# Kernel optimization log

Hardware: AMD Instinct MI355X
Metric: run time of the kernel (lower is better)

Reference implementation:

```python
import jax, jax.numpy as jnp
import numpy as np
from jax.scipy.special import logsumexp

T, B, H, K = 256, 256, 512, 64


def setup_inputs() -> dict:
    key = jax.random.key(0)
    k1, k2, k3, k4, k5, k6, k7, k8 = jax.random.split(key, 8)
    hiddens = jax.random.normal(k1, (T, B, H), dtype=jnp.float32)
    lens = jax.random.randint(k2, (B,), 1, T + 1)              # sentence lengths in [1, T]
    tags = jax.random.randint(k3, (T, B), 0, K)                # gold tags
    W = jax.random.normal(k4, (K, H), dtype=jnp.float32) * (1.0 / np.sqrt(H))
    b = jax.random.normal(k5, (K,), dtype=jnp.float32) * 0.01
    begin_transition = jax.random.normal(k6, (K,), dtype=jnp.float32)
    transition = jax.random.normal(k7, (K, K), dtype=jnp.float32)
    end_transition = jax.random.normal(k8, (K,), dtype=jnp.float32)
    return {"hiddens": hiddens, "lens": lens, "tags": tags, "W": W, "b": b,
            "begin_transition": begin_transition, "transition": transition,
            "end_transition": end_transition}


def reference(hiddens, lens, tags, W, b, begin_transition, transition, end_transition):
    # emissions: [T, B, K] = hidden2emission(hiddens)
    em = jnp.einsum('tbh,kh->tbk', hiddens, W) + b
    t_len, batch, k = em.shape

    # ---- forward (partition) score: log-semiring DP over time ----
    alpha0 = em[0] + begin_transition                       # [B, K]

    def step(alpha, e_t):
        # alpha_t[b, j] = logsumexp_i(alpha[b, i] + transition[j, i]) + e_t[b, j]
        a = logsumexp(alpha[:, None, :] + transition[None, :, :], axis=-1) + e_t
        return a, a

    _, alphas = jax.lax.scan(step, alpha0, em[1:])          # [T-1, B, K]
    alphas = jnp.concatenate([alpha0[None], alphas], axis=0)  # [T, B, K]

    bidx = jnp.arange(batch)
    last_alpha = alphas[lens - 1, bidx]                     # [B, K] at each sentence end
    forward_score = logsumexp(last_alpha + end_transition, axis=-1)  # [B]

    # ---- gold path score ----
    em_g = jnp.take_along_axis(em, tags[:, :, None], axis=-1)[..., 0]   # [T, B]
    inc = transition[tags[1:], tags[:-1]] + em_g[1:]                     # [T-1, B]
    first = (begin_transition[tags[0]] + em_g[0])[None]                  # [1, B]
    scores = jnp.cumsum(jnp.concatenate([first, inc], axis=0), axis=0)   # [T, B]
    last_scores = scores[lens - 1, bidx]                                 # [B]
    last_tags = tags[lens - 1, bidx]
    gold_score = last_scores + end_transition[last_tags]                 # [B]

    return jnp.sum(forward_score - gold_score)
```

## Files before the change

kernel.cpp:

```cpp
#include <hip/hip_runtime.h>
#include <hip/hip_bf16.h>
#include <math.h>

#define T_DIM 256
#define B_DIM 256
#define H_DIM 512
#define K_DIM 64
#define LN2F 0.69314718055994531f

typedef __attribute__((ext_vector_type(8))) short bfrag_t;
typedef __attribute__((ext_vector_type(4))) float f4_t;

__device__ inline bfrag_t pack8(float4 a, float4 b) {
  union { bfrag_t v; __hip_bfloat162 h[4]; } u;
  u.h[0] = __float22bfloat162_rn(float2{a.x, a.y});
  u.h[1] = __float22bfloat162_rn(float2{a.z, a.w});
  u.h[2] = __float22bfloat162_rn(float2{b.x, b.y});
  u.h[3] = __float22bfloat162_rn(float2{b.z, b.w});
  return u.v;
}

__global__ __launch_bounds__(256) void wconv(const float* __restrict__ W,
                                             short* __restrict__ Wb,
                                             float* __restrict__ out) {
  if (blockIdx.x == 0 && threadIdx.x == 0) *out = 0.f;
  const int i = (blockIdx.x * 256 + threadIdx.x) * 8;
  const float4 a = *(const float4*)(W + i);
  const float4 b = *(const float4*)(W + i + 4);
  *(bfrag_t*)(Wb + i) = pack8(a, b);
}

__global__ __launch_bounds__(256, 4) void emis_gemm10(
    const float* __restrict__ hid,
    const short* __restrict__ Wb,
    const float* __restrict__ bias,
    const int*   __restrict__ tags,
    short* __restrict__ emPb,
    float* __restrict__ goldRaw)
{
  __shared__ __hip_bfloat16 AsH[2][64 * 72];
  float* Cs = (float*)&AsH[0][0];

  const int tid  = threadIdx.x;
  const int wv   = tid >> 6;
  const int lane = tid & 63;
  const int l16  = lane & 15;
  const int quad = lane >> 4;
  const int m0   = blockIdx.x * 64;

  const short* wb = Wb + ((wv * 16 + l16) * H_DIM + quad * 8);

  const int sr = tid >> 2;
  const int sc = (tid & 3) << 4;
  const float* hrow = hid + (size_t)(m0 + sr) * H_DIM + sc;

  f4_t acc[4];
#pragma unroll
  for (int mt = 0; mt < 4; ++mt) acc[mt] = (f4_t){0.f, 0.f, 0.f, 0.f};

  float4 p0 = *(const float4*)(hrow + 0);
  float4 p1 = *(const float4*)(hrow + 4);
  float4 p2 = *(const float4*)(hrow + 8);
  float4 p3 = *(const float4*)(hrow + 12);
  bfrag_t bc0 = *(const bfrag_t*)(wb + 0);
  bfrag_t bc1 = *(const bfrag_t*)(wb + 32);
  *(bfrag_t*)(&AsH[0][sr * 72 + sc + 0]) = pack8(p0, p1);
  *(bfrag_t*)(&AsH[0][sr * 72 + sc + 8]) = pack8(p2, p3);
  __syncthreads();

#pragma unroll
  for (int it = 0; it < 8; ++it) {
    bfrag_t bn0, bn1;
    if (it < 7) {
      p0 = *(const float4*)(hrow + (it + 1) * 64 + 0);
      p1 = *(const float4*)(hrow + (it + 1) * 64 + 4);
      p2 = *(const float4*)(hrow + (it + 1) * 64 + 8);
      p3 = *(const float4*)(hrow + (it + 1) * 64 + 12);
      bn0 = *(const bfrag_t*)(wb + (it + 1) * 64);
      bn1 = *(const bfrag_t*)(wb + (it + 1) * 64 + 32);
    }
#pragma unroll
    for (int kc2 = 0; kc2 < 2; ++kc2) {
      const bfrag_t bf = kc2 ? bc1 : bc0;
#pragma unroll
      for (int mt = 0; mt < 4; ++mt) {
        const bfrag_t af =
            *(const bfrag_t*)(&AsH[it & 1][(mt * 16 + l16) * 72 + kc2 * 32 + quad * 8]);
        acc[mt] = __builtin_amdgcn_mfma_f32_16x16x32_bf16(af, bf, acc[mt], 0, 0, 0);
      }
    }
    if (it < 7) {
      *(bfrag_t*)(&AsH[(it + 1) & 1][sr * 72 + sc + 0]) = pack8(p0, p1);
      *(bfrag_t*)(&AsH[(it + 1) & 1][sr * 72 + sc + 8]) = pack8(p2, p3);
      bc0 = bn0; bc1 = bn1;
    }
    __syncthreads();
  }

  const float bn = bias[wv * 16 + l16];
#pragma unroll
  for (int mt = 0; mt < 4; ++mt)
#pragma unroll
    for (int r = 0; r < 4; ++r)
      Cs[(mt * 16 + quad * 4 + r) * 68 + wv * 16 + l16] = acc[mt][r] + bn;
  __syncthreads();

  const int t  = m0 >> 8;
  const int b0 = m0 & 255;
  if (tid < 64) {
    const int tg = tags[t * B_DIM + b0 + tid];
    goldRaw[t * B_DIM + b0 + tid] = Cs[tid * 68 + tg];
  }

  const int g0 = b0 >> 4;
  const int bl = tid & 15;
  const int qq = (tid >> 4) & 3;
  const int gl = tid >> 6;
#pragma unroll
  for (int i2 = 0; i2 < 2; ++i2) {
    float4 v0 = *(const float4*)(&Cs[(gl * 16 + bl) * 68 + (i2 * 2 + 0) * 16 + qq * 4]);
    float4 v1 = *(const float4*)(&Cs[(gl * 16 + bl) * 68 + (i2 * 2 + 1) * 16 + qq * 4]);
    v0.x = __expf(v0.x); v0.y = __expf(v0.y); v0.z = __expf(v0.z); v0.w = __expf(v0.w);
    v1.x = __expf(v1.x); v1.y = __expf(v1.y); v1.z = __expf(v1.z); v1.w = __expf(v1.w);
    const size_t off = ((((size_t)(g0 + gl) * 256 + t) * 64 + qq * 16 + bl) << 4) + i2 * 8;
    *(bfrag_t*)(emPb + off) = pack8(v0, v1);
  }
}

__global__ __launch_bounds__(128, 1) void crf_dp10(
    const short* __restrict__ emPb,
    const float* __restrict__ goldRaw,
    const int* __restrict__ lens,
    const int* __restrict__ tags,
    const float* __restrict__ trans,
    const float* __restrict__ beginT,
    const float* __restrict__ endT,
    float* __restrict__ out)
{
  const int g    = blockIdx.x;
  const int tid  = threadIdx.x;
  const int wv   = tid >> 6;
  const int lane = tid & 63;
  const int n    = lane & 15;
  const int q    = lane >> 4;
  const int b    = g * 16 + n;

  __shared__ float xs[64 * 16];
  __shared__ int   Lxs[64];
  __shared__ float s0d[16];
  __shared__ int   Ls0[16];
  __shared__ float gpart;

  const int len = lens[b];
  const int cap = len - 1;
  const short* base = emPb + (((size_t)g * 256) * 64 + lane) * 16;

  float eend[16];
#pragma unroll
  for (int k = 0; k < 16; ++k)
    eend[k] = __expf(endT[(k >> 2) * 16 + q * 4 + (k & 3)]);

  float y[16];
  int Lint = 0;
  bfrag_t bf0, bf1;
  bfrag_t wA0, wA1, wB0, wB1, wC0, wC1, wD0, wD1;
  bfrag_t wE0, wE1, wF0, wF1, wG0, wG1, wH0, wH1;
  float g0 = 0.f;

#define LOADW(D0, D1, t) { \
    D0 = *(const bfrag_t*)(base + (size_t)(t) * 1024 + 0); \
    D1 = *(const bfrag_t*)(base + (size_t)(t) * 1024 + 8); }

#define CVT16(DST, S0, S1) { \
    union { bfrag_t v; __hip_bfloat162 h[4]; } _c0, _c1; \
    _c0.v = (S0); _c1.v = (S1); \
    float2 _f; \
    _f = __bfloat1622float2(_c0.h[0]); DST[0] = _f.x; DST[1] = _f.y; \
    _f = __bfloat1622float2(_c0.h[1]); DST[2] = _f.x; DST[3] = _f.y; \
    _f = __bfloat1622float2(_c0.h[2]); DST[4] = _f.x; DST[5] = _f.y; \
    _f = __bfloat1622float2(_c0.h[3]); DST[6] = _f.x; DST[7] = _f.y; \
    _f = __bfloat1622float2(_c1.h[0]); DST[8] = _f.x; DST[9] = _f.y; \
    _f = __bfloat1622float2(_c1.h[1]); DST[10] = _f.x; DST[11] = _f.y; \
    _f = __bfloat1622float2(_c1.h[2]); DST[12] = _f.x; DST[13] = _f.y; \
    _f = __bfloat1622float2(_c1.h[3]); DST[14] = _f.x; DST[15] = _f.y; }

#define RESCALE() { \
    float _m0 = fmaxf(fmaxf(y[0], y[1]), fmaxf(y[2], y[3])); \
    float _m1 = fmaxf(fmaxf(y[4], y[5]), fmaxf(y[6], y[7])); \
    float _m2 = fmaxf(fmaxf(y[8], y[9]), fmaxf(y[10], y[11])); \
    float _m3 = fmaxf(fmaxf(y[12], y[13]), fmaxf(y[14], y[15])); \
    float _mx = fmaxf(fmaxf(_m0, _m1), fmaxf(_m2, _m3)); \
    _mx = fmaxf(_mx, __shfl_xor(_mx, 16)); \
    _mx = fmaxf(_mx, __shfl_xor(_mx, 32)); \
    int _e; (void)frexpf(_mx, &_e); \
    Lint += _e; \
    _Pragma("unroll") for (int k = 0; k < 16; ++k) y[k] = ldexpf(y[k], -_e); }

#define BUILDBV(S) { \
    union { bfrag_t v; __hip_bfloat162 h[4]; } _u0, _u1; \
    _u0.h[0] = __float22bfloat162_rn(float2{S[0], S[1]}); \
    _u0.h[1] = __float22bfloat162_rn(float2{S[2], S[3]}); \
    _u0.h[2] = __float22bfloat162_rn(float2{S[4], S[5]}); \
    _u0.h[3] = __float22bfloat162_rn(float2{S[6], S[7]}); \
    _u1.h[0] = __float22bfloat162_rn(float2{S[8], S[9]}); \
    _u1.h[1] = __float22bfloat162_rn(float2{S[10], S[11]}); \
    _u1.h[2] = __float22bfloat162_rn(float2{S[12], S[13]}); \
    _u1.h[3] = __float22bfloat162_rn(float2{S[14], S[15]}); \
    bf0 = _u0.v; bf1 = _u1.v; }

  const f4_t zro = (f4_t){0.f, 0.f, 0.f, 0.f};

  if (wv == 0) {
    bfrag_t aE[8];
#pragma unroll
    for (int jt = 0; jt < 4; ++jt)
#pragma unroll
      for (int kt = 0; kt < 2; ++kt) {
        union { bfrag_t v; __hip_bfloat16 h[8]; } u;
#pragma unroll
        for (int r = 0; r < 8; ++r) {
          const int i = (2 * kt + (r >> 2)) * 16 + q * 4 + (r & 3);
          u.h[r] = __float2bfloat16(__expf(trans[(jt * 16 + n) * K_DIM + i]));
        }
        aE[jt * 2 + kt] = u.v;
      }

    float snap[16];
    int Lsnap = 0;
    LOADW(wA0, wA1, 0);
    {
      float w0[16];
      CVT16(w0, wA0, wA1);
#pragma unroll
      for (int k = 0; k < 16; ++k) {
        const int j = (k >> 2) * 16 + q * 4 + (k & 3);
        y[k] = w0[k] * __expf(beginT[j]);
        snap[k] = (cap == 0) ? y[k] : 0.0f;
      }
    }
    RESCALE(); BUILDBV(y);
    LOADW(wA0, wA1, 1); LOADW(wB0, wB1, 2); LOADW(wC0, wC1, 3); LOADW(wD0, wD1, 4);
    LOADW(wE0, wE1, 5); LOADW(wF0, wF1, 6); LOADW(wG0, wG1, 7); LOADW(wH0, wH1, 8);

#define STEPF(T, W0, W1, RSC) { \
    float _w[16]; \
    CVT16(_w, W0, W1); \
    f4_t _a0 = __builtin_amdgcn_mfma_f32_16x16x32_bf16(aE[0], bf0, zro, 0, 0, 0); \
    f4_t _a1 = __builtin_amdgcn_mfma_f32_16x16x32_bf16(aE[2], bf0, zro, 0, 0, 0); \
    f4_t _a2 = __builtin_amdgcn_mfma_f32_16x16x32_bf16(aE[4], bf0, zro, 0, 0, 0); \
    f4_t _a3 = __builtin_amdgcn_mfma_f32_16x16x32_bf16(aE[6], bf0, zro, 0, 0, 0); \
    _a0 = __builtin_amdgcn_mfma_f32_16x16x32_bf16(aE[1], bf1, _a0, 0, 0, 0); \
    _a1 = __builtin_amdgcn_mfma_f32_16x16x32_bf16(aE[3], bf1, _a1, 0, 0, 0); \
    _a2 = __builtin_amdgcn_mfma_f32_16x16x32_bf16(aE[5], bf1, _a2, 0, 0, 0); \
    _a3 = __builtin_amdgcn_mfma_f32_16x16x32_bf16(aE[7], bf1, _a3, 0, 0, 0); \
    _Pragma("unroll") for (int r = 0; r < 4; ++r) { \
      y[r]      = _a0[r] * _w[r]; \
      y[4 + r]  = _a1[r] * _w[4 + r]; \
      y[8 + r]  = _a2[r] * _w[8 + r]; \
      y[12 + r] = _a3[r] * _w[12 + r]; } \
    const bool _hit = ((T) == cap); \
    _Pragma("unroll") for (int k = 0; k < 16; ++k) snap[k] = _hit ? y[k] : snap[k]; \
    Lsnap = _hit ? Lint : Lsnap; \
    if (RSC) { RESCALE(); } \
    BUILDBV(y); }

    int t = 1;
    for (int it = 0; it < 15; ++it, t += 8) {
      STEPF(t + 0, wA0, wA1, 0); LOADW(wA0, wA1, t + 8);
      STEPF(t + 1, wB0, wB1, 0); LOADW(wB0, wB1, t + 9);
      STEPF(t + 2, wC0, wC1, 1); LOADW(wC0, wC1, t + 10);
      STEPF(t + 3, wD0, wD1, 0); LOADW(wD0, wD1, t + 11);
      STEPF(t + 4, wE0, wE1, 0); LOADW(wE0, wE1, t + 12);
      STEPF(t + 5, wF0, wF1, 0); LOADW(wF0, wF1, t + 13);
      STEPF(t + 6, wG0, wG1, 1); LOADW(wG0, wG1, t + 14);
      STEPF(t + 7, wH0, wH1, 0); LOADW(wH0, wH1, t + 15);
    }
    STEPF(121, wA0, wA1, 0); STEPF(122, wB0, wB1, 0); STEPF(123, wC0, wC1, 1);
    STEPF(124, wD0, wD1, 0); STEPF(125, wE0, wE1, 0); STEPF(126, wF0, wF1, 0);
    STEPF(127, wG0, wG1, 0);

#pragma unroll
    for (int k = 0; k < 16; ++k) xs[lane * 16 + k] = y[k];
    Lxs[lane] = Lint;
    float sd = 0.f;
#pragma unroll
    for (int k = 0; k < 16; ++k) sd += snap[k] * eend[k];
    sd += __shfl_xor(sd, 16);
    sd += __shfl_xor(sd, 32);
    if (lane < 16) { s0d[lane] = sd; Ls0[lane] = Lsnap; }

    for (int c = 0; c < 32; ++c) {
      const int tt = q + 4 * c;
      if (tt < len) {
        const int tg = tags[(size_t)tt * B_DIM + b];
        float v = goldRaw[(size_t)tt * B_DIM + b];
        v += (tt == 0) ? beginT[tg]
                       : trans[(size_t)tg * K_DIM + tags[(size_t)(tt - 1) * B_DIM + b]];
        if (tt == cap) v += endT[tg];
        g0 += v;
      }
    }
    float gr = g0;
#pragma unroll
    for (int o = 1; o < 64; o <<= 1) gr += __shfl_xor(gr, o);
    if (lane == 0) gpart = gr;
  } else {
    bfrag_t aET[8];
#pragma unroll
    for (int jt = 0; jt < 4; ++jt)
#pragma unroll
      for (int kt = 0; kt < 2; ++kt) {
        union { bfrag_t v; __hip_bfloat16 h[8]; } u;
#pragma unroll
        for (int r = 0; r < 8; ++r) {
          const int i = (2 * kt + (r >> 2)) * 16 + q * 4 + (r & 3);
          u.h[r] = __float2bfloat16(__expf(trans[(size_t)i * K_DIM + (jt * 16 + n)]));
        }
        aET[jt * 2 + kt] = u.v;
      }

#pragma unroll
    for (int k = 0; k < 16; ++k) y[k] = 0.f;
    LOADW(wA0, wA1, 255); LOADW(wB0, wB1, 254); LOADW(wC0, wC1, 253); LOADW(wD0, wD1, 252);
    LOADW(wE0, wE1, 251); LOADW(wF0, wF1, 250); LOADW(wG0, wG1, 249); LOADW(wH0, wH1, 248);

#define STEPB(T, W0, W1, RSC) { \
    float _w[16]; \
    CVT16(_w, W0, W1); \
    const bool _hit = ((T) == cap); \
    float _d[16]; \
    _Pragma("unroll") for (int k = 0; k < 16; ++k) \
      _d[k] = (_hit ? eend[k] : y[k]) * _w[k]; \
    BUILDBV(_d); \
    f4_t _a0 = __builtin_amdgcn_mfma_f32_16x16x32_bf16(aET[0], bf0, zro, 0, 0, 0); \
    f4_t _a1 = __builtin_amdgcn_mfma_f32_16x16x32_bf16(aET[2], bf0, zro, 0, 0, 0); \
    f4_t _a2 = __builtin_amdgcn_mfma_f32_16x16x32_bf16(aET[4], bf0, zro, 0, 0, 0); \
    f4_t _a3 = __builtin_amdgcn_mfma_f32_16x16x32_bf16(aET[6], bf0, zro, 0, 0, 0); \
    _a0 = __builtin_amdgcn_mfma_f32_16x16x32_bf16(aET[1], bf1, _a0, 0, 0, 0); \
    _a1 = __builtin_amdgcn_mfma_f32_16x16x32_bf16(aET[3], bf1, _a1, 0, 0, 0); \
    _a2 = __builtin_amdgcn_mfma_f32_16x16x32_bf16(aET[5], bf1, _a2, 0, 0, 0); \
    _a3 = __builtin_amdgcn_mfma_f32_16x16x32_bf16(aET[7], bf1, _a3, 0, 0, 0); \
    _Pragma("unroll") for (int r = 0; r < 4; ++r) { \
      y[r]      = _a0[r]; \
      y[4 + r]  = _a1[r]; \
      y[8 + r]  = _a2[r]; \
      y[12 + r] = _a3[r]; } \
    if (RSC) { RESCALE(); } }

    int t = 255;
    for (int it = 0; it < 16; ++it, t -= 8) {
      STEPB(t - 0, wA0, wA1, 0); LOADW(wA0, wA1, t - 8);
      STEPB(t - 1, wB0, wB1, 0); LOADW(wB0, wB1, t - 9);
      STEPB(t - 2, wC0, wC1, 1); LOADW(wC0, wC1, t - 10);
      STEPB(t - 3, wD0, wD1, 0); LOADW(wD0, wD1, t - 11);
      STEPB(t - 4, wE0, wE1, 0); LOADW(wE0, wE1, t - 12);
      STEPB(t - 5, wF0, wF1, 0); LOADW(wF0, wF1, t - 13);
      STEPB(t - 6, wG0, wG1, 1); LOADW(wG0, wG1, t - 14);
      STEPB(t - 7, wH0, wH1, 0); LOADW(wH0, wH1, t - 15);
    }

    for (int c = 0; c < 32; ++c) {
      const int tt = 128 + q + 4 * c;
      if (tt < len) {
        const int tg = tags[(size_t)tt * B_DIM + b];
        float v = goldRaw[(size_t)tt * B_DIM + b];
        v += trans[(size_t)tg * K_DIM + tags[(size_t)(tt - 1) * B_DIM + b]];
        if (tt == cap) v += endT[tg];
        g0 += v;
      }
    }
  }

  __syncthreads();

  if (wv == 1) {
    float dot1 = 0.f;
#pragma unroll
    for (int k = 0; k < 16; ++k) dot1 += xs[lane * 16 + k] * y[k];
    dot1 += __shfl_xor(dot1, 16);
    dot1 += __shfl_xor(dot1, 32);

    const bool hi = (cap >= 128);
    const float dsel = hi ? dot1 : s0d[n];
    const float Lsel = (float)(hi ? (Lxs[lane] + Lint) : Ls0[n]);
    const float f = __logf(dsel) + Lsel * LN2F;

    float r = 0.25f * f - g0;
#pragma unroll
    for (int o = 1; o < 64; o <<= 1) r += __shfl_xor(r, o);
    if (lane == 0) atomicAdd(out, r - gpart);
  }
}

extern "C" void kernel_launch(void* const* d_in, const int* in_sizes, int n_in,
                              void* d_out, int out_size, void* d_ws, size_t ws_size,
                              hipStream_t stream) {
  const float* hiddens = (const float*)d_in[0];
  const int*   lens    = (const int*)  d_in[1];
  const int*   tags    = (const int*)  d_in[2];
  const float* W       = (const float*)d_in[3];
  const float* bias    = (const float*)d_in[4];
  const float* beginT  = (const float*)d_in[5];
  const float* trans   = (const float*)d_in[6];
  const float* endT    = (const float*)d_in[7];

  short* emPb    = (short*)d_ws;
  float* goldRaw = (float*)(emPb + (size_t)16 * 256 * 64 * 16);
  short* Wb      = (short*)(goldRaw + B_DIM * T_DIM);
  float* out     = (float*)d_out;

  wconv<<<(K_DIM * H_DIM) / (256 * 8), 256, 0, stream>>>(W, Wb, out);
  emis_gemm10<<<(T_DIM * B_DIM) / 64, 256, 0, stream>>>(hiddens, Wb, bias, tags, emPb, goldRaw);
  crf_dp10<<<16, 128, 0, stream>>>(emPb, goldRaw, lens, tags, trans, beginT, endT, out);
}
```

Baseline: 253.1 us.

## Interleave two batch groups per CRF DP block to hide MFMA latency

Each DP block now handles two 16-sentence groups, with their forward and backward recurrences interleaved, and the grid is halved from 16 to 8 blocks. The two independent dependency chains let MFMA and conversion latency of one chain overlap with work on the other. The end-of-sentence snapshot moves from a per-step register select into a conditional shared-memory store, and the prefetch depth drops from 8 to 4 steps per chain. In exchange the kernel uses fewer CUs, needs more registers per thread, and does twice the serial gold-score work per wave.

```diff
diff --git a/kernel.cpp b/kernel.cpp
--- a/kernel.cpp
+++ b/kernel.cpp
@@ -127,7 +127,7 @@
   }
 }
 
-__global__ __launch_bounds__(128, 1) void crf_dp10(
+__global__ __launch_bounds__(128, 1) void crf_dp11(
     const short* __restrict__ emPb,
     const float* __restrict__ goldRaw,
     const int* __restrict__ lens,
@@ -143,33 +143,33 @@
   const int lane = tid & 63;
   const int n    = lane & 15;
   const int q    = lane >> 4;
-  const int b    = g * 16 + n;
-
-  __shared__ float xs[64 * 16];
-  __shared__ int   Lxs[64];
-  __shared__ float s0d[16];
-  __shared__ int   Ls0[16];
+  const int b0   = g * 32 + n;
+  const int b1   = b0 + 16;
+
+  __shared__ float xs[2 * 64 * 16];
+  __shared__ float snapL[2 * 64 * 16];
+  __shared__ int   Lxs[2 * 64];
+  __shared__ float s0d[2 * 16];
+  __shared__ int   Ls0[2 * 16];
   __shared__ float gpart;
 
-  const int len = lens[b];
-  const int cap = len - 1;
-  const short* base = emPb + (((size_t)g * 256) * 64 + lane) * 16;
-
-  float eend[16];
-#pragma unroll
-  for (int k = 0; k < 16; ++k)
-    eend[k] = __expf(endT[(k >> 2) * 16 + q * 4 + (k & 3)]);
-
-  float y[16];
-  int Lint = 0;
-  bfrag_t bf0, bf1;
-  bfrag_t wA0, wA1, wB0, wB1, wC0, wC1, wD0, wD1;
-  bfrag_t wE0, wE1, wF0, wF1, wG0, wG1, wH0, wH1;
+  const int len0 = lens[b0], cap0 = len0 - 1;
+  const int len1 = lens[b1], cap1 = len1 - 1;
+  const short* base0 = emPb + (((size_t)(2 * g)     * 256) * 64 + lane) * 16;
+  const short* base1 = emPb + (((size_t)(2 * g + 1) * 256) * 64 + lane) * 16;
+  float* snp0 = &snapL[(0 * 64 + lane) * 16];
+  float* snp1 = &snapL[(1 * 64 + lane) * 16];
+
+  float y0[16], y1[16];
+  int Lint0 = 0, Lint1 = 0, Lsnap0 = 0, Lsnap1 = 0;
+  bfrag_t xb0, xb1, zb0, zb1;
+  bfrag_t fA0,fA1,fB0,fB1,fC0,fC1,fD0,fD1;
+  bfrag_t gA0,gA1,gB0,gB1,gC0,gC1,gD0,gD1;
   float g0 = 0.f;
 
-#define LOADW(D0, D1, t) { \
-    D0 = *(const bfrag_t*)(base + (size_t)(t) * 1024 + 0); \
-    D1 = *(const bfrag_t*)(base + (size_t)(t) * 1024 + 8); }
+#define LOADW(D0, D1, BASE, t) { \
+    D0 = *(const bfrag_t*)((BASE) + (size_t)(t) * 1024 + 0); \
+    D1 = *(const bfrag_t*)((BASE) + (size_t)(t) * 1024 + 8); }
 
 #define CVT16(DST, S0, S1) { \
     union { bfrag_t v; __hip_bfloat162 h[4]; } _c0, _c1; \
@@ -184,19 +184,19 @@
     _f = __bfloat1622float2(_c1.h[2]); DST[12] = _f.x; DST[13] = _f.y; \
     _f = __bfloat1622float2(_c1.h[3]); DST[14] = _f.x; DST[15] = _f.y; }
 
-#define RESCALE() { \
-    float _m0 = fmaxf(fmaxf(y[0], y[1]), fmaxf(y[2], y[3])); \
-    float _m1 = fmaxf(fmaxf(y[4], y[5]), fmaxf(y[6], y[7])); \
-    float _m2 = fmaxf(fmaxf(y[8], y[9]), fmaxf(y[10], y[11])); \
-    float _m3 = fmaxf(fmaxf(y[12], y[13]), fmaxf(y[14], y[15])); \
+#define RESCALE(Y, LINT) { \
+    float _m0 = fmaxf(fmaxf(Y[0], Y[1]), fmaxf(Y[2], Y[3])); \
+    float _m1 = fmaxf(fmaxf(Y[4], Y[5]), fmaxf(Y[6], Y[7])); \
+    float _m2 = fmaxf(fmaxf(Y[8], Y[9]), fmaxf(Y[10], Y[11])); \
+    float _m3 = fmaxf(fmaxf(Y[12], Y[13]), fmaxf(Y[14], Y[15])); \
     float _mx = fmaxf(fmaxf(_m0, _m1), fmaxf(_m2, _m3)); \
     _mx = fmaxf(_mx, __shfl_xor(_mx, 16)); \
     _mx = fmaxf(_mx, __shfl_xor(_mx, 32)); \
     int _e; (void)frexpf(_mx, &_e); \
-    Lint += _e; \
-    _Pragma("unroll") for (int k = 0; k < 16; ++k) y[k] = ldexpf(y[k], -_e); }
-
-#define BUILDBV(S) { \
+    LINT += _e; \
+    _Pragma("unroll") for (int _k = 0; _k < 16; ++_k) Y[_k] = ldexpf(Y[_k], -_e); }
+
+#define BUILDBV(S, B0, B1) { \
     union { bfrag_t v; __hip_bfloat162 h[4]; } _u0, _u1; \
     _u0.h[0] = __float22bfloat162_rn(float2{S[0], S[1]}); \
     _u0.h[1] = __float22bfloat162_rn(float2{S[2], S[3]}); \
@@ -206,7 +206,13 @@
     _u1.h[1] = __float22bfloat162_rn(float2{S[10], S[11]}); \
     _u1.h[2] = __float22bfloat162_rn(float2{S[12], S[13]}); \
     _u1.h[3] = __float22bfloat162_rn(float2{S[14], S[15]}); \
-    bf0 = _u0.v; bf1 = _u1.v; }
+    B0 = _u0.v; B1 = _u1.v; }
+
+#define SNAPW(SNP, Y) { \
+    ((f4_t*)(SNP))[0] = (f4_t){Y[0], Y[1], Y[2], Y[3]}; \
+    ((f4_t*)(SNP))[1] = (f4_t){Y[4], Y[5], Y[6], Y[7]}; \
+    ((f4_t*)(SNP))[2] = (f4_t){Y[8], Y[9], Y[10], Y[11]}; \
+    ((f4_t*)(SNP))[3] = (f4_t){Y[12], Y[13], Y[14], Y[15]}; }
 
   const f4_t zro = (f4_t){0.f, 0.f, 0.f, 0.f};
 
@@ -225,78 +231,105 @@
         aE[jt * 2 + kt] = u.v;
       }
 
-    float snap[16];
-    int Lsnap = 0;
-    LOADW(wA0, wA1, 0);
-    {
-      float w0[16];
-      CVT16(w0, wA0, wA1);
-#pragma unroll
-      for (int k = 0; k < 16; ++k) {
-        const int j = (k >> 2) * 16 + q * 4 + (k & 3);
-        y[k] = w0[k] * __expf(beginT[j]);
-        snap[k] = (cap == 0) ? y[k] : 0.0f;
-      }
-    }
-    RESCALE(); BUILDBV(y);
-    LOADW(wA0, wA1, 1); LOADW(wB0, wB1, 2); LOADW(wC0, wC1, 3); LOADW(wD0, wD1, 4);
-    LOADW(wE0, wE1, 5); LOADW(wF0, wF1, 6); LOADW(wG0, wG1, 7); LOADW(wH0, wH1, 8);
-
-#define STEPF(T, W0, W1, RSC) { \
+#define STEPF(T, Y, BB0, BB1, W0, W1, CAP, LINT, LSNAP, SNP, RSC) { \
     float _w[16]; \
     CVT16(_w, W0, W1); \
-    f4_t _a0 = __builtin_amdgcn_mfma_f32_16x16x32_bf16(aE[0], bf0, zro, 0, 0, 0); \
-    f4_t _a1 = __builtin_amdgcn_mfma_f32_16x16x32_bf16(aE[2], bf0, zro, 0, 0, 0); \
-    f4_t _a2 = __builtin_amdgcn_mfma_f32_16x16x32_bf16(aE[4], bf0, zro, 0, 0, 0); \
-    f4_t _a3 = __builtin_amdgcn_mfma_f32_16x16x32_bf16(aE[6], bf0, zro, 0, 0, 0); \
-    _a0 = __builtin_amdgcn_mfma_f32_16x16x32_bf16(aE[1], bf1, _a0, 0, 0, 0); \
-    _a1 = __builtin_amdgcn_mfma_f32_16x16x32_bf16(aE[3], bf1, _a1, 0, 0, 0); \
-    _a2 = __builtin_amdgcn_mfma_f32_16x16x32_bf16(aE[5], bf1, _a2, 0, 0, 0); \
-    _a3 = __builtin_amdgcn_mfma_f32_16x16x32_bf16(aE[7], bf1, _a3, 0, 0, 0); \
-    _Pragma("unroll") for (int r = 0; r < 4; ++r) { \
-      y[r]      = _a0[r] * _w[r]; \
-      y[4 + r]  = _a1[r] * _w[4 + r]; \
-      y[8 + r]  = _a2[r] * _w[8 + r]; \
-      y[12 + r] = _a3[r] * _w[12 + r]; } \
-    const bool _hit = ((T) == cap); \
-    _Pragma("unroll") for (int k = 0; k < 16; ++k) snap[k] = _hit ? y[k] : snap[k]; \
-    Lsnap = _hit ? Lint : Lsnap; \
-    if (RSC) { RESCALE(); } \
-    BUILDBV(y); }
-
-    int t = 1;
-    for (int it = 0; it < 15; ++it, t += 8) {
-      STEPF(t + 0, wA0, wA1, 0); LOADW(wA0, wA1, t + 8);
-      STEPF(t + 1, wB0, wB1, 0); LOADW(wB0, wB1, t + 9);
-      STEPF(t + 2, wC0, wC1, 1); LOADW(wC0, wC1, t + 10);
-      STEPF(t + 3, wD0, wD1, 0); LOADW(wD0, wD1, t + 11);
-      STEPF(t + 4, wE0, wE1, 0); LOADW(wE0, wE1, t + 12);
-      STEPF(t + 5, wF0, wF1, 0); LOADW(wF0, wF1, t + 13);
-      STEPF(t + 6, wG0, wG1, 1); LOADW(wG0, wG1, t + 14);
-      STEPF(t + 7, wH0, wH1, 0); LOADW(wH0, wH1, t + 15);
-    }
-    STEPF(121, wA0, wA1, 0); STEPF(122, wB0, wB1, 0); STEPF(123, wC0, wC1, 1);
-    STEPF(124, wD0, wD1, 0); STEPF(125, wE0, wE1, 0); STEPF(126, wF0, wF1, 0);
-    STEPF(127, wG0, wG1, 0);
-
-#pragma unroll
-    for (int k = 0; k < 16; ++k) xs[lane * 16 + k] = y[k];
-    Lxs[lane] = Lint;
-    float sd = 0.f;
-#pragma unroll
-    for (int k = 0; k < 16; ++k) sd += snap[k] * eend[k];
-    sd += __shfl_xor(sd, 16);
-    sd += __shfl_xor(sd, 32);
-    if (lane < 16) { s0d[lane] = sd; Ls0[lane] = Lsnap; }
-
-    for (int c = 0; c < 32; ++c) {
+    f4_t _a0 = __builtin_amdgcn_mfma_f32_16x16x32_bf16(aE[0], BB0, zro, 0, 0, 0); \
+    f4_t _a1 = __builtin_amdgcn_mfma_f32_16x16x32_bf16(aE[2], BB0, zro, 0, 0, 0); \
+    f4_t _a2 = __builtin_amdgcn_mfma_f32_16x16x32_bf16(aE[4], BB0, zro, 0, 0, 0); \
+    f4_t _a3 = __builtin_amdgcn_mfma_f32_16x16x32_bf16(aE[6], BB0, zro, 0, 0, 0); \
+    _a0 = __builtin_amdgcn_mfma_f32_16x16x32_bf16(aE[1], BB1, _a0, 0, 0, 0); \
+    _a1 = __builtin_amdgcn_mfma_f32_16x16x32_bf16(aE[3], BB1, _a1, 0, 0, 0); \
+    _a2 = __builtin_amdgcn_mfma_f32_16x16x32_bf16(aE[5], BB1, _a2, 0, 0, 0); \
+    _a3 = __builtin_amdgcn_mfma_f32_16x16x32_bf16(aE[7], BB1, _a3, 0, 0, 0); \
+    _Pragma("unroll") for (int _r = 0; _r < 4; ++_r) { \
+      Y[_r]      = _a0[_r] * _w[_r]; \
+      Y[4 + _r]  = _a1[_r] * _w[4 + _r]; \
+      Y[8 + _r]  = _a2[_r] * _w[8 + _r]; \
+      Y[12 + _r] = _a3[_r] * _w[12 + _r]; } \
+    if ((T) == (CAP)) { LSNAP = (LINT); SNAPW(SNP, Y); } \
+    if (RSC) { RESCALE(Y, LINT); } \
+    BUILDBV(Y, BB0, BB1); }
+
+#pragma unroll
+    for (int k = 0; k < 4; ++k) { ((f4_t*)snp0)[k] = zro; ((f4_t*)snp1)[k] = zro; }
+
+    LOADW(fA0, fA1, base0, 0); LOADW(gA0, gA1, base1, 0);
+    {
+      float w0x[16], w0z[16], ebT[16];
+      CVT16(w0x, fA0, fA1); CVT16(w0z, gA0, gA1);
+#pragma unroll
+      for (int k = 0; k < 16; ++k)
+        ebT[k] = __expf(beginT[(k >> 2) * 16 + q * 4 + (k & 3)]);
+#pragma unroll
+      for (int k = 0; k < 16; ++k) { y0[k] = w0x[k] * ebT[k]; y1[k] = w0z[k] * ebT[k]; }
+      if (cap0 == 0) { Lsnap0 = 0; SNAPW(snp0, y0); }
+      if (cap1 == 0) { Lsnap1 = 0; SNAPW(snp1, y1); }
+    }
+    RESCALE(y0, Lint0); RESCALE(y1, Lint1);
+    BUILDBV(y0, xb0, xb1); BUILDBV(y1, zb0, zb1);
+    LOADW(fA0, fA1, base0, 1); LOADW(gA0, gA1, base1, 1);
+    LOADW(fB0, fB1, base0, 2); LOADW(gB0, gB1, base1, 2);
+    LOADW(fC0, fC1, base0, 3); LOADW(gC0, gC1, base1, 3);
+    LOADW(fD0, fD1, base0, 4); LOADW(gD0, gD1, base1, 4);
+
+    for (int it = 0; it < 31; ++it) {
+      const int t = 1 + 4 * it;
+      STEPF(t + 0, y0, xb0, xb1, fA0, fA1, cap0, Lint0, Lsnap0, snp0, 0);
+      STEPF(t + 0, y1, zb0, zb1, gA0, gA1, cap1, Lint1, Lsnap1, snp1, 0);
+      LOADW(fA0, fA1, base0, t + 4); LOADW(gA0, gA1, base1, t + 4);
+      STEPF(t + 1, y0, xb0, xb1, fB0, fB1, cap0, Lint0, Lsnap0, snp0, 0);
+      STEPF(t + 1, y1, zb0, zb1, gB0, gB1, cap1, Lint1, Lsnap1, snp1, 0);
+      LOADW(fB0, fB1, base0, t + 5); LOADW(gB0, gB1, base1, t + 5);
+      STEPF(t + 2, y0, xb0, xb1, fC0, fC1, cap0, Lint0, Lsnap0, snp0, 1);
+      STEPF(t + 2, y1, zb0, zb1, gC0, gC1, cap1, Lint1, Lsnap1, snp1, 1);
+      LOADW(fC0, fC1, base0, t + 6); LOADW(gC0, gC1, base1, t + 6);
+      STEPF(t + 3, y0, xb0, xb1, fD0, fD1, cap0, Lint0, Lsnap0, snp0, 0);
+      STEPF(t + 3, y1, zb0, zb1, gD0, gD1, cap1, Lint1, Lsnap1, snp1, 0);
+      LOADW(fD0, fD1, base0, t + 7); LOADW(gD0, gD1, base1, t + 7);
+    }
+    STEPF(125, y0, xb0, xb1, fA0, fA1, cap0, Lint0, Lsnap0, snp0, 0);
+    STEPF(125, y1, zb0, zb1, gA0, gA1, cap1, Lint1, Lsnap1, snp1, 0);
+    STEPF(126, y0, xb0, xb1, fB0, fB1, cap0, Lint0, Lsnap0, snp0, 0);
+    STEPF(126, y1, zb0, zb1, gB0, gB1, cap1, Lint1, Lsnap1, snp1, 0);
+    STEPF(127, y0, xb0, xb1, fC0, fC1, cap0, Lint0, Lsnap0, snp0, 0);
+    STEPF(127, y1, zb0, zb1, gC0, gC1, cap1, Lint1, Lsnap1, snp1, 0);
+
+#pragma unroll
+    for (int k = 0; k < 16; ++k) {
+      xs[(0 * 64 + lane) * 16 + k] = y0[k];
+      xs[(1 * 64 + lane) * 16 + k] = y1[k];
+    }
+    Lxs[0 * 64 + lane] = Lint0;
+    Lxs[1 * 64 + lane] = Lint1;
+    {
+      float eend[16];
+#pragma unroll
+      for (int k = 0; k < 16; ++k)
+        eend[k] = __expf(endT[(k >> 2) * 16 + q * 4 + (k & 3)]);
+      float sd0 = 0.f, sd1 = 0.f;
+#pragma unroll
+      for (int k = 0; k < 16; ++k) { sd0 += snp0[k] * eend[k]; sd1 += snp1[k] * eend[k]; }
+      sd0 += __shfl_xor(sd0, 16); sd0 += __shfl_xor(sd0, 32);
+      sd1 += __shfl_xor(sd1, 16); sd1 += __shfl_xor(sd1, 32);
+      if (lane < 16) {
+        s0d[lane] = sd0;      Ls0[lane] = Lsnap0;
+        s0d[16 + lane] = sd1; Ls0[16 + lane] = Lsnap1;
+      }
+    }
+
+    for (int cc = 0; cc < 64; ++cc) {
+      const int ch = cc >> 5;
+      const int c  = cc & 31;
       const int tt = q + 4 * c;
-      if (tt < len) {
-        const int tg = tags[(size_t)tt * B_DIM + b];
-        float v = goldRaw[(size_t)tt * B_DIM + b];
+      const int bb   = ch ? b1 : b0;
+      const int lenc = ch ? len1 : len0;
+      if (tt < lenc) {
+        const int tg = tags[(size_t)tt * B_DIM + bb];
+        float v = goldRaw[(size_t)tt * B_DIM + bb];
         v += (tt == 0) ? beginT[tg]
-                       : trans[(size_t)tg * K_DIM + tags[(size_t)(tt - 1) * B_DIM + b]];
-        if (tt == cap) v += endT[tg];
+                       : trans[(size_t)tg * K_DIM + tags[(size_t)(tt - 1) * B_DIM + bb]];
+        if (tt == lenc - 1) v += endT[tg];
         g0 += v;
       }
     }
@@ -319,53 +352,69 @@
         aET[jt * 2 + kt] = u.v;
       }
 
-#pragma unroll
-    for (int k = 0; k < 16; ++k) y[k] = 0.f;
-    LOADW(wA0, wA1, 255); LOADW(wB0, wB1, 254); LOADW(wC0, wC1, 253); LOADW(wD0, wD1, 252);
-    LOADW(wE0, wE1, 251); LOADW(wF0, wF1, 250); LOADW(wG0, wG1, 249); LOADW(wH0, wH1, 248);
-
-#define STEPB(T, W0, W1, RSC) { \
+    float eend[16];
+#pragma unroll
+    for (int k = 0; k < 16; ++k)
+      eend[k] = __expf(endT[(k >> 2) * 16 + q * 4 + (k & 3)]);
+
+#define STEPB(T, Y, W0, W1, CAP, LINT, RSC) { \
     float _w[16]; \
     CVT16(_w, W0, W1); \
-    const bool _hit = ((T) == cap); \
+    const bool _hit = ((T) == (CAP)); \
     float _d[16]; \
-    _Pragma("unroll") for (int k = 0; k < 16; ++k) \
-      _d[k] = (_hit ? eend[k] : y[k]) * _w[k]; \
-    BUILDBV(_d); \
-    f4_t _a0 = __builtin_amdgcn_mfma_f32_16x16x32_bf16(aET[0], bf0, zro, 0, 0, 0); \
-    f4_t _a1 = __builtin_amdgcn_mfma_f32_16x16x32_bf16(aET[2], bf0, zro, 0, 0, 0); \
-    f4_t _a2 = __builtin_amdgcn_mfma_f32_16x16x32_bf16(aET[4], bf0, zro, 0, 0, 0); \
-    f4_t _a3 = __builtin_amdgcn_mfma_f32_16x16x32_bf16(aET[6], bf0, zro, 0, 0, 0); \
-    _a0 = __builtin_amdgcn_mfma_f32_16x16x32_bf16(aET[1], bf1, _a0, 0, 0, 0); \
-    _a1 = __builtin_amdgcn_mfma_f32_16x16x32_bf16(aET[3], bf1, _a1, 0, 0, 0); \
-    _a2 = __builtin_amdgcn_mfma_f32_16x16x32_bf16(aET[5], bf1, _a2, 0, 0, 0); \
-    _a3 = __builtin_amdgcn_mfma_f32_16x16x32_bf16(aET[7], bf1, _a3, 0, 0, 0); \
-    _Pragma("unroll") for (int r = 0; r < 4; ++r) { \
-      y[r]      = _a0[r]; \
-      y[4 + r]  = _a1[r]; \
-      y[8 + r]  = _a2[r]; \
-      y[12 + r] = _a3[r]; } \
-    if (RSC) { RESCALE(); } }
-
-    int t = 255;
-    for (int it = 0; it < 16; ++it, t -= 8) {
-      STEPB(t - 0, wA0, wA1, 0); LOADW(wA0, wA1, t - 8);
-      STEPB(t - 1, wB0, wB1, 0); LOADW(wB0, wB1, t - 9);
-      STEPB(t - 2, wC0, wC1, 1); LOADW(wC0, wC1, t - 10);
-      STEPB(t - 3, wD0, wD1, 0); LOADW(wD0, wD1, t - 11);
-      STEPB(t - 4, wE0, wE1, 0); LOADW(wE0, wE1, t - 12);
-      STEPB(t - 5, wF0, wF1, 0); LOADW(wF0, wF1, t - 13);
-      STEPB(t - 6, wG0, wG1, 1); LOADW(wG0, wG1, t - 14);
-      STEPB(t - 7, wH0, wH1, 0); LOADW(wH0, wH1, t - 15);
-    }
-
-    for (int c = 0; c < 32; ++c) {
+    _Pragma("unroll") for (int _k = 0; _k < 16; ++_k) \
+      _d[_k] = (_hit ? eend[_k] : Y[_k]) * _w[_k]; \
+    bfrag_t _b0, _b1; \
+    BUILDBV(_d, _b0, _b1); \
+    f4_t _a0 = __builtin_amdgcn_mfma_f32_16x16x32_bf16(aET[0], _b0, zro, 0, 0, 0); \
+    f4_t _a1 = __builtin_amdgcn_mfma_f32_16x16x32_bf16(aET[2], _b0, zro, 0, 0, 0); \
+    f4_t _a2 = __builtin_amdgcn_mfma_f32_16x16x32_bf16(aET[4], _b0, zro, 0, 0, 0); \
+    f4_t _a3 = __builtin_amdgcn_mfma_f32_16x16x32_bf16(aET[6], _b0, zro, 0, 0, 0); \
+    _a0 = __builtin_amdgcn_mfma_f32_16x16x32_bf16(aET[1], _b1, _a0, 0, 0, 0); \
+    _a1 = __builtin_amdgcn_mfma_f32_16x16x32_bf16(aET[3], _b1, _a1, 0, 0, 0); \
+    _a2 = __builtin_amdgcn_mfma_f32_16x16x32_bf16(aET[5], _b1, _a2, 0, 0, 0); \
+    _a3 = __builtin_amdgcn_mfma_f32_16x16x32_bf16(aET[7], _b1, _a3, 0, 0, 0); \
+    _Pragma("unroll") for (int _r = 0; _r < 4; ++_r) { \
+      Y[_r]      = _a0[_r]; \
+      Y[4 + _r]  = _a1[_r]; \
+      Y[8 + _r]  = _a2[_r]; \
+      Y[12 + _r] = _a3[_r]; } \
+    if (RSC) { RESCALE(Y, LINT); } }
+
+#pragma unroll
+    for (int k = 0; k < 16; ++k) { y0[k] = 0.f; y1[k] = 0.f; }
+    LOADW(fA0, fA1, base0, 255); LOADW(gA0, gA1, base1, 255);
+    LOADW(fB0, fB1, base0, 254); LOADW(gB0, gB1, base1, 254);
+    LOADW(fC0, fC1, base0, 253); LOADW(gC0, gC1, base1, 253);
+    LOADW(fD0, fD1, base0, 252); LOADW(gD0, gD1, base1, 252);
+
+    for (int it = 0; it < 32; ++it) {
+      const int t = 255 - 4 * it;
+      STEPB(t - 0, y0, fA0, fA1, cap0, Lint0, 0);
+      STEPB(t - 0, y1, gA0, gA1, cap1, Lint1, 0);
+      LOADW(fA0, fA1, base0, t - 4); LOADW(gA0, gA1, base1, t - 4);
+      STEPB(t - 1, y0, fB0, fB1, cap0, Lint0, 0);
+      STEPB(t - 1, y1, gB0, gB1, cap1, Lint1, 0);
+      LOADW(fB0, fB1, base0, t - 5); LOADW(gB0, gB1, base1, t - 5);
+      STEPB(t - 2, y0, fC0, fC1, cap0, Lint0, 1);
+      STEPB(t - 2, y1, gC0, gC1, cap1, Lint1, 1);
+      LOADW(fC0, fC1, base0, t - 6); LOADW(gC0, gC1, base1, t - 6);
+      STEPB(t - 3, y0, fD0, fD1, cap0, Lint0, 0);
+      STEPB(t - 3, y1, gD0, gD1, cap1, Lint1, 0);
+      LOADW(fD0, fD1, base0, t - 7); LOADW(gD0, gD1, base1, t - 7);
+    }
+
+    for (int cc = 0; cc < 64; ++cc) {
+      const int ch = cc >> 5;
+      const int c  = cc & 31;
       const int tt = 128 + q + 4 * c;
-      if (tt < len) {
-        const int tg = tags[(size_t)tt * B_DIM + b];
-        float v = goldRaw[(size_t)tt * B_DIM + b];
-        v += trans[(size_t)tg * K_DIM + tags[(size_t)(tt - 1) * B_DIM + b]];
-        if (tt == cap) v += endT[tg];
+      const int bb   = ch ? b1 : b0;
+      const int lenc = ch ? len1 : len0;
+      if (tt < lenc) {
+        const int tg = tags[(size_t)tt * B_DIM + bb];
+        float v = goldRaw[(size_t)tt * B_DIM + bb];
+        v += trans[(size_t)tg * K_DIM + tags[(size_t)(tt - 1) * B_DIM + bb]];
+        if (tt == lenc - 1) v += endT[tg];
         g0 += v;
       }
     }
@@ -374,16 +423,21 @@
   __syncthreads();
 
   if (wv == 1) {
-    float dot1 = 0.f;
-#pragma unroll
-    for (int k = 0; k < 16; ++k) dot1 += xs[lane * 16 + k] * y[k];
-    dot1 += __shfl_xor(dot1, 16);
-    dot1 += __shfl_xor(dot1, 32);
-
-    const bool hi = (cap >= 128);
-    const float dsel = hi ? dot1 : s0d[n];
-    const float Lsel = (float)(hi ? (Lxs[lane] + Lint) : Ls0[n]);
-    const float f = __logf(dsel) + Lsel * LN2F;
+    float d0 = 0.f, d1 = 0.f;
+#pragma unroll
+    for (int k = 0; k < 16; ++k) {
+      d0 += xs[(0 * 64 + lane) * 16 + k] * y0[k];
+      d1 += xs[(1 * 64 + lane) * 16 + k] * y1[k];
+    }
+    d0 += __shfl_xor(d0, 16); d0 += __shfl_xor(d0, 32);
+    d1 += __shfl_xor(d1, 16); d1 += __shfl_xor(d1, 32);
+
+    const bool hi0 = (cap0 >= 128), hi1 = (cap1 >= 128);
+    const float ds0 = hi0 ? d0 : s0d[n];
+    const float ds1 = hi1 ? d1 : s0d[16 + n];
+    const float L0 = (float)(hi0 ? (Lxs[lane] + Lint0) : Ls0[n]);
+    const float L1 = (float)(hi1 ? (Lxs[64 + lane] + Lint1) : Ls0[16 + n]);
+    const float f = (__logf(ds0) + L0 * LN2F) + (__logf(ds1) + L1 * LN2F);
 
     float r = 0.25f * f - g0;
 #pragma unroll
@@ -411,5 +465,5 @@
 
   wconv<<<(K_DIM * H_DIM) / (256 * 8), 256, 0, stream>>>(W, Wb, out);
   emis_gemm10<<<(T_DIM * B_DIM) / 64, 256, 0, stream>>>(hiddens, Wb, bias, tags, emPb, goldRaw);
-  crf_dp10<<<16, 128, 0, stream>>>(emPb, goldRaw, lens, tags, trans, beginT, endT, out);
+  crf_dp11<<<8, 128, 0, stream>>>(emPb, goldRaw, lens, tags, trans, beginT, endT, out);
 }
```

Result: slower. 284.2 us (+12.3%).
